# Kernel tuning notes

Hardware: AMD Instinct MI355X
Metric: run time of the kernel (lower is better)

## Reference

```python
import jax, jax.numpy as jnp
import numpy as np

N = 50000   # nodes
E = 600000  # edges
R = 8       # relations
B = 8       # bases
D = 128     # feature dim (in = hidden = out)
H = 4       # GAT heads
NEG = 0.1   # leaky_relu slope between layers
LN_EPS = 1e-5


def layer_norm(x, g, b):
    mu = jnp.mean(x, axis=-1, keepdims=True)
    var = jnp.mean(jnp.square(x - mu), axis=-1, keepdims=True)
    return (x - mu) * jax.lax.rsqrt(var + LN_EPS) * g + b


def rgcn(x, basis, comp, root, bias, src, dst, etype):
    # W[r] = sum_b comp[r,b] * basis[b]  -> [R, D, D]
    W = jnp.einsum('rb,bio->rio', comp, basis)
    h = jnp.einsum('ni,rio->rno', x, W)          # [R, N, D] per-relation transform
    msg = h[etype, src]                          # [E, D] gather per edge
    seg = etype.astype(jnp.int32) * N + dst      # (relation, dst) segment id
    deg = jax.ops.segment_sum(jnp.ones((src.shape[0],), x.dtype), seg, num_segments=R * N)
    inv = 1.0 / jnp.maximum(deg, 1.0)            # mean aggregation per relation
    out = jax.ops.segment_sum(msg * inv[seg][:, None], dst, num_segments=N)
    return out + x @ root + bias


def gat(x, W, a_src, a_dst, bias, src, dst):
    h = (x @ W).reshape(N, H, D)                 # [N, H, D]
    loop = jnp.arange(N, dtype=src.dtype)        # add self loops
    s2 = jnp.concatenate([src, loop])
    d2 = jnp.concatenate([dst, loop])
    hs = h[s2]                                   # [E+N, H, D]
    e = jnp.sum(hs * a_src, -1) + jnp.sum(h[d2] * a_dst, -1)   # [E+N, H]
    e = jax.nn.leaky_relu(e, 0.2)
    m = jax.ops.segment_max(e, d2, num_segments=N)              # stable softmax per dst
    ex = jnp.exp(e - m[d2])
    denom = jax.ops.segment_sum(ex, d2, num_segments=N)
    coef = ex / denom[d2]                        # [E+N, H]
    out = jax.ops.segment_sum(coef[..., None] * hs, d2, num_segments=N)  # [N, H, D]
    return jnp.mean(out, axis=1) + bias          # concat=False -> head mean


def setup_inputs():
    key = jax.random.key(0)
    ks = jax.random.split(key, 20)
    nrm = lambda k, shp, s=0.1: jax.random.normal(k, shp, dtype=jnp.float32) * s
    inp = {
        'x': jax.random.normal(ks[0], (N, D), dtype=jnp.float32),
        'edge_index': jax.random.randint(ks[1], (2, E), 0, N, dtype=jnp.int32),
        'edge_type': jax.random.randint(ks[2], (E,), 0, R, dtype=jnp.int32),
        'r0_basis': nrm(ks[3], (B, D, D)), 'r0_comp': nrm(ks[4], (R, B)),
        'r0_root': nrm(ks[5], (D, D)), 'r0_bias': jnp.zeros((D,), jnp.float32),
        'ln0_g': jnp.ones((D,), jnp.float32), 'ln0_b': jnp.zeros((D,), jnp.float32),
        'r1_basis': nrm(ks[6], (B, D, D)), 'r1_comp': nrm(ks[7], (R, B)),
        'r1_root': nrm(ks[8], (D, D)), 'r1_bias': jnp.zeros((D,), jnp.float32),
        'ln1_g': jnp.ones((D,), jnp.float32), 'ln1_b': jnp.zeros((D,), jnp.float32),
        'gat_w': nrm(ks[9], (D, H * D)), 'gat_asrc': nrm(ks[10], (H, D)),
        'gat_adst': nrm(ks[11], (H, D)), 'gat_bias': jnp.zeros((D,), jnp.float32),
        'ln2_g': jnp.ones((D,), jnp.float32), 'ln2_b': jnp.zeros((D,), jnp.float32),
        'r2_basis': nrm(ks[12], (B, D, D)), 'r2_comp': nrm(ks[13], (R, B)),
        'r2_root': nrm(ks[14], (D, D)), 'r2_bias': jnp.zeros((D,), jnp.float32),
    }
    return inp


def reference(x, edge_index, edge_type,
              r0_basis, r0_comp, r0_root, r0_bias, ln0_g, ln0_b,
              r1_basis, r1_comp, r1_root, r1_bias, ln1_g, ln1_b,
              gat_w, gat_asrc, gat_adst, gat_bias, ln2_g, ln2_b,
              r2_basis, r2_comp, r2_root, r2_bias):
    src, dst = edge_index[0], edge_index[1]
    h = rgcn(x, r0_basis, r0_comp, r0_root, r0_bias, src, dst, edge_type)
    h = jax.nn.leaky_relu(layer_norm(h, ln0_g, ln0_b), NEG)
    h = rgcn(h, r1_basis, r1_comp, r1_root, r1_bias, src, dst, edge_type)
    h = jax.nn.leaky_relu(layer_norm(h, ln1_g, ln1_b), NEG)
    h = gat(h, gat_w, gat_asrc, gat_adst, gat_bias, src, dst)
    h = jax.nn.leaky_relu(layer_norm(h, ln2_g, ln2_b), NEG)
    h = rgcn(h, r2_basis, r2_comp, r2_root, r2_bias, src, dst, edge_type)
    # F.normalize(p=2, dim=1)
    return h / jnp.maximum(jnp.linalg.norm(h, axis=1, keepdims=True), 1e-12)
```

## Files before the change

### kernel.cpp

```cpp
#include <hip/hip_runtime.h>
#include <hip/hip_bf16.h>

#define DD 128
#define NKEY8 8
#define LDA_AGG 1056
#define SRCM 0x00FFFFFF

using bf16x8 = __attribute__((ext_vector_type(8))) __bf16;
using f32x4  = __attribute__((ext_vector_type(4))) float;

__device__ __forceinline__ float leaky(float x, float s){ return x > 0.f ? x : s * x; }
__device__ __forceinline__ float bflo(unsigned u){ return __uint_as_float(u << 16); }
__device__ __forceinline__ float bfhi(unsigned u){ return __uint_as_float(u & 0xffff0000u); }
__device__ __forceinline__ unsigned bfpack(float x, float y){
  __hip_bfloat16 hx = __float2bfloat16(x), hy = __float2bfloat16(y);
  unsigned short ux = *reinterpret_cast<unsigned short*>(&hx);
  unsigned short uy = *reinterpret_cast<unsigned short*>(&hy);
  return (unsigned)ux | ((unsigned)uy << 16);
}

__global__ void k_hist(const int* __restrict__ dst, const int* __restrict__ et,
                       int* __restrict__ cnt, int E_){
  int e = blockIdx.x * 256 + threadIdx.x;
  if (e < E_) atomicAdd(&cnt[dst[e] * NKEY8 + et[e]], 1);
}

__global__ void k_scan1(const int* __restrict__ cnt, int* __restrict__ ptr,
                        int* __restrict__ part, int n){
  __shared__ int sm[256];
  int tid = threadIdx.x;
  int base = blockIdx.x * 1024 + tid * 4;
  int a0 = base + 0 < n ? cnt[base + 0] : 0;
  int a1 = base + 1 < n ? cnt[base + 1] : 0;
  int a2 = base + 2 < n ? cnt[base + 2] : 0;
  int a3 = base + 3 < n ? cnt[base + 3] : 0;
  int s = a0 + a1 + a2 + a3;
  sm[tid] = s; __syncthreads();
  for (int off = 1; off < 256; off <<= 1){
    int v = tid >= off ? sm[tid - off] : 0;
    __syncthreads(); sm[tid] += v; __syncthreads();
  }
  int ex = sm[tid] - s;
  if (tid == 255) part[blockIdx.x] = sm[255];
  if (base + 0 < n) ptr[base + 0] = ex;
  if (base + 1 < n) ptr[base + 1] = ex + a0;
  if (base + 2 < n) ptr[base + 2] = ex + a0 + a1;
  if (base + 3 < n) ptr[base + 3] = ex + a0 + a1 + a2;
}

__global__ void k_scan2(int* __restrict__ part, int nb){
  __shared__ int sm[512];
  int tid = threadIdx.x;
  int v = tid < nb ? part[tid] : 0;
  sm[tid] = v; __syncthreads();
  for (int off = 1; off < 512; off <<= 1){
    int u = tid >= off ? sm[tid - off] : 0;
    __syncthreads(); sm[tid] += u; __syncthreads();
  }
  if (tid < nb) part[tid] = sm[tid] - v;
}

__global__ void k_scan3(int* __restrict__ ptr, const int* __restrict__ part, int n, int E_){
  int i = blockIdx.x * 256 + threadIdx.x;
  if (i < n) ptr[i] += part[i >> 10];
  if (i == n) ptr[n] = E_;
}

__global__ void k_inv(const int* __restrict__ ptr, float* __restrict__ inv, int n){
  int i = blockIdx.x * 256 + threadIdx.x;
  if (i < n) inv[i] = 1.0f / fmaxf((float)(ptr[i + 1] - ptr[i]), 1.0f);
}

__global__ void k_scatter_pos(const int* __restrict__ src, const int* __restrict__ dst,
                              const int* __restrict__ et, int* __restrict__ run,
                              int* __restrict__ epk, int E_){
  int e = blockIdx.x * 256 + threadIdx.x;
  if (e >= E_) return;
  int r = et[e];
  int pos = atomicAdd(&run[dst[e] * NKEY8 + r], 1);
  epk[pos] = (r << 24) | src[e];
}

__global__ void k_cvt(const float* __restrict__ in, __hip_bfloat16* __restrict__ out, int n){
  int i = blockIdx.x * 256 + threadIdx.x;
  if (i < n) out[i] = __float2bfloat16(in[i]);
}

__global__ void k_makeW(const float* __restrict__ basis, const float* __restrict__ comp,
                        const float* __restrict__ root, __hip_bfloat16* __restrict__ Wp){
  int idx = blockIdx.x * 256 + threadIdx.x;
  int k = idx >> 7, n = idx & 127;
  float v;
  if (k < 1024){
    int r = k >> 7, i = k & 127;
    float s = 0.f;
    #pragma unroll
    for (int b = 0; b < 8; b++) s += comp[r * 8 + b] * basis[b * 16384 + i * 128 + n];
    v = s;
  } else {
    v = root[(k - 1024) * 128 + n];
  }
  int kt = k >> 5, kr = k & 31;
  int lane = (n & 15) | ((kr >> 3) << 4);
  int ii = kr & 7, nt = n >> 4;
  Wp[((size_t)(kt * 8 + nt) * 64 + lane) * 8 + ii] = __float2bfloat16(v);
}

__global__ void k_packGZ(const float* __restrict__ Wg, __hip_bfloat16* __restrict__ Wp){
  int idx = blockIdx.x * 256 + threadIdx.x;
  int k = idx >> 7, n = idx & 127;
  int h = k >> 7, i = k & 127;
  float v = Wg[(size_t)i * 512 + h * 128 + n];
  int kt = k >> 5, kr = k & 31;
  int lane = (n & 15) | ((kr >> 3) << 4);
  int ii = kr & 7, nt = n >> 4;
  Wp[((size_t)(kt * 8 + nt) * 64 + lane) * 8 + ii] = __float2bfloat16(v);
}

__global__ void k_valpha(const float* __restrict__ Wg, const float* __restrict__ a_src,
                         const float* __restrict__ a_dst, float* __restrict__ vT){
  int id = blockIdx.x * 256 + threadIdx.x;
  int sd = id >> 9, h = (id >> 7) & 3, i = id & 127;
  const float* a = (sd ? a_dst : a_src) + h * 128;
  const float* w = Wg + (size_t)i * 512 + h * 128;
  float s = 0.f;
  #pragma unroll 4
  for (int o = 0; o < 128; o++) s += w[o] * a[o];
  vT[(size_t)sd * 512 + h * 128 + i] = s;
}

__global__ void k_av(const __hip_bfloat16* __restrict__ xb, const float* __restrict__ vT,
                     float* __restrict__ aS, float* __restrict__ aD, int N_){
  int node = blockIdx.x * 4 + (threadIdx.x >> 6);
  if (node >= N_) return;
  int lane = threadIdx.x & 63;
  int h = lane >> 4, dg = lane & 15;
  uint4 u = *(const uint4*)(xb + (size_t)node * DD + dg * 8);
  const float* vs = vT + h * 128 + dg * 8;
  const float* vd = vT + 512 + h * 128 + dg * 8;
  float ss = 0.f, sd = 0.f;
  #pragma unroll
  for (int w = 0; w < 4; w++){
    unsigned uw = ((const unsigned*)&u)[w];
    float f0 = bflo(uw), f1 = bfhi(uw);
    ss += f0 * vs[w * 2] + f1 * vs[w * 2 + 1];
    sd += f0 * vd[w * 2] + f1 * vd[w * 2 + 1];
  }
  for (int o = 1; o < 16; o <<= 1){ ss += __shfl_xor(ss, o); sd += __shfl_xor(sd, o); }
  if (dg == 0){ aS[(size_t)node * 4 + h] = ss; aD[(size_t)node * 4 + h] = sd; }
}

__global__ void k_csr_agg(const int* __restrict__ ptr, const int* __restrict__ epk,
                          const float* __restrict__ inv, const __hip_bfloat16* __restrict__ xb,
                          __hip_bfloat16* __restrict__ agg, int N_){
  int w = threadIdx.x >> 6, lane = threadIdx.x & 63;
  int t = blockIdx.x * 4 + w;
  if (t >= N_) return;
  int beg = ptr[t * 8], end = ptr[t * 8 + 8];
  const __hip_bfloat16* xcol = xb + lane * 2;
  __hip_bfloat16* aggrow = agg + (size_t)t * LDA_AGG + lane * 2;
  const float* invrow = inv + (size_t)t * 8;
  float a0 = 0.f, a1 = 0.f;
  int cur = -1;
  unsigned written = 0;

#define CSR_FLUSH() { float iv = invrow[cur]; \
    *(unsigned*)(aggrow + cur * 128) = bfpack(a0 * iv, a1 * iv); \
    written |= (1u << cur); }
#define CSR_PROC(PK, U) { int r_ = (PK) >> 24; \
    if (r_ != cur){ if (cur >= 0){ CSR_FLUSH(); } cur = r_; a0 = 0.f; a1 = 0.f; } \
    a0 += bflo(U); a1 += bfhi(U); }

  int e = beg;
  for (; e + 4 <= end; e += 4){
    int pk0 = epk[e], pk1 = epk[e + 1], pk2 = epk[e + 2], pk3 = epk[e + 3];
    unsigned u0 = *(const unsigned*)(xcol + (size_t)(pk0 & SRCM) * DD);
    unsigned u1 = *(const unsigned*)(xcol + (size_t)(pk1 & SRCM) * DD);
    unsigned u2 = *(const unsigned*)(xcol + (size_t)(pk2 & SRCM) * DD);
    unsigned u3 = *(const unsigned*)(xcol + (size_t)(pk3 & SRCM) * DD);
    CSR_PROC(pk0, u0); CSR_PROC(pk1, u1); CSR_PROC(pk2, u2); CSR_PROC(pk3, u3);
  }
  for (; e < end; e++){
    int pk0 = epk[e];
    unsigned u0 = *(const unsigned*)(xcol + (size_t)(pk0 & SRCM) * DD);
    CSR_PROC(pk0, u0);
  }
  if (cur >= 0){ CSR_FLUSH(); }
  #pragma unroll
  for (int r = 0; r < 8; r++)
    if (!(written & (1u << r))) *(unsigned*)(aggrow + r * 128) = 0u;
#undef CSR_PROC
#undef CSR_FLUSH
}

__global__ void k_zagg(const int* __restrict__ ptr, const int* __restrict__ epk,
                       const float* __restrict__ cf, const float* __restrict__ cfS,
                       const float* __restrict__ den, const __hip_bfloat16* __restrict__ xb,
                       __hip_bfloat16* __restrict__ z, int N_){
  int w = threadIdx.x >> 6, lane = threadIdx.x & 63;
  int t = blockIdx.x * 4 + w;
  if (t >= N_) return;
  int dg = lane & 31, ep = lane >> 5;
  int beg = ptr[t * 8], end = ptr[t * 8 + 8];
  float acc[4][4];
  #pragma unroll
  for (int h = 0; h < 4; h++)
    #pragma unroll
    for (int j = 0; j < 4; j++) acc[h][j] = 0.f;
  const __hip_bfloat16* xbase = xb + dg * 4;
  for (int e = beg + ep; e < end; e += 2){
    int s = epk[e] & SRCM;
    uint2 v = *(const uint2*)(xbase + (size_t)s * DD);
    float4 c = *(const float4*)(cf + (size_t)e * 4);
    float f0 = bflo(v.x), f1 = bfhi(v.x), f2 = bflo(v.y), f3 = bfhi(v.y);
    const float* cp = (const float*)&c;
    #pragma unroll
    for (int h = 0; h < 4; h++){
      acc[h][0] += cp[h] * f0; acc[h][1] += cp[h] * f1;
      acc[h][2] += cp[h] * f2; acc[h][3] += cp[h] * f3;
    }
  }
  #pragma unroll
  for (int h = 0; h < 4; h++)
    #pragma unroll
    for (int j = 0; j < 4; j++) acc[h][j] += __shfl_xor(acc[h][j], 32);
  if (ep == 0){
    uint2 v = *(const uint2*)(xbase + (size_t)t * DD);
    float f0 = bflo(v.x), f1 = bfhi(v.x), f2 = bflo(v.y), f3 = bfhi(v.y);
    float4 cs = *(const float4*)(cfS + (size_t)t * 4);
    float4 dn = *(const float4*)(den + (size_t)t * 4);
    const float* csp = (const float*)&cs;
    const float* dnp = (const float*)&dn;
    #pragma unroll
    for (int h = 0; h < 4; h++){
      float sc = 0.25f / dnp[h];
      float y0 = (acc[h][0] + csp[h] * f0) * sc;
      float y1 = (acc[h][1] + csp[h] * f1) * sc;
      float y2 = (acc[h][2] + csp[h] * f2) * sc;
      float y3 = (acc[h][3] + csp[h] * f3) * sc;
      uint2 o; o.x = bfpack(y0, y1); o.y = bfpack(y2, y3);
      *(uint2*)(z + (size_t)t * 512 + h * 128 + dg * 4) = o;
    }
  }
}

template<int MODE>
__launch_bounds__(256)
__global__ void k_gemm_mfma(const __hip_bfloat16* __restrict__ A1, int lda1, int K1,
                            const __hip_bfloat16* __restrict__ A2, int K2,
                            int M, const __hip_bfloat16* __restrict__ Bp, int ntt,
                            const float* __restrict__ bias,
                            const float* __restrict__ ln_g, const float* __restrict__ ln_b,
                            float* __restrict__ Cf, __hip_bfloat16* __restrict__ Cb,
                            int ldc){
  int wave = threadIdx.x >> 6, lane = threadIdx.x & 63;
  int nt0 = blockIdx.y << 3;
  int mbase = blockIdx.x * 128 + wave * 32;
  int r0 = min(mbase + (lane & 15), M - 1);
  int r1 = min(mbase + 16 + (lane & 15), M - 1);
  int koff = (lane >> 4) << 3;
  f32x4 acc[2][8];
  #pragma unroll
  for (int i = 0; i < 2; i++)
    #pragma unroll
    for (int j = 0; j < 8; j++) acc[i][j] = (f32x4){0.f, 0.f, 0.f, 0.f};

  int ktile = 0;
  {
    const __hip_bfloat16* a0p = A1 + (size_t)r0 * lda1 + koff;
    const __hip_bfloat16* a1p = A1 + (size_t)r1 * lda1 + koff;
    for (int k0 = 0; k0 < K1; k0 += 32, ++ktile){
      bf16x8 a0 = *(const bf16x8*)(a0p + k0);
      bf16x8 a1 = *(const bf16x8*)(a1p + k0);
      const bf16x8* bfr = (const bf16x8*)(Bp + (((size_t)ktile * ntt + nt0) * 64 + lane) * 8);
      #pragma unroll
      for (int nt = 0; nt < 8; nt++){
        bf16x8 b = bfr[(size_t)nt * 64];
        acc[0][nt] = __builtin_amdgcn_mfma_f32_16x16x32_bf16(a0, b, acc[0][nt], 0, 0, 0);
        acc[1][nt] = __builtin_amdgcn_mfma_f32_16x16x32_bf16(a1, b, acc[1][nt], 0, 0, 0);
      }
    }
  }
  if (A2){
    const __hip_bfloat16* a0p = A2 + (size_t)r0 * DD + koff;
    const __hip_bfloat16* a1p = A2 + (size_t)r1 * DD + koff;
    for (int k0 = 0; k0 < K2; k0 += 32, ++ktile){
      bf16x8 a0 = *(const bf16x8*)(a0p + k0);
      bf16x8 a1 = *(const bf16x8*)(a1p + k0);
      const bf16x8* bfr = (const bf16x8*)(Bp + (((size_t)ktile * ntt + nt0) * 64 + lane) * 8);
      #pragma unroll
      for (int nt = 0; nt < 8; nt++){
        bf16x8 b = bfr[(size_t)nt * 64];
        acc[0][nt] = __builtin_amdgcn_mfma_f32_16x16x32_bf16(a0, b, acc[0][nt], 0, 0, 0);
        acc[1][nt] = __builtin_amdgcn_mfma_f32_16x16x32_bf16(a1, b, acc[1][nt], 0, 0, 0);
      }
    }
  }

  const int colb = lane & 15;
  const int lq = lane >> 4;

  float bias8[8], g8[8], b8[8];
  #pragma unroll
  for (int nt = 0; nt < 8; nt++){
    int c = (nt << 4) + colb;
    bias8[nt] = bias ? bias[c] : 0.f;
    if (MODE == 1){ g8[nt] = ln_g[c]; b8[nt] = ln_b[c]; }
  }

  #pragma unroll
  for (int mt = 0; mt < 2; mt++){
    #pragma unroll
    for (int j = 0; j < 4; j++){
      int row = mbase + mt * 16 + lq * 4 + j;
      if (MODE == 1){
        float v[8]; float s = 0.f;
        #pragma unroll
        for (int nt = 0; nt < 8; nt++){ v[nt] = acc[mt][nt][j] + bias8[nt]; s += v[nt]; }
        #pragma unroll
        for (int o = 1; o < 16; o <<= 1) s += __shfl_xor(s, o);
        float mu = s * (1.f / 128.f);
        float q = 0.f;
        #pragma unroll
        for (int nt = 0; nt < 8; nt++){ float dd = v[nt] - mu; q += dd * dd; }
        #pragma unroll
        for (int o = 1; o < 16; o <<= 1) q += __shfl_xor(q, o);
        float rstd = rsqrtf(q * (1.f / 128.f) + 1e-5f);
        if (row < M){
          #pragma unroll
          for (int nt = 0; nt < 8; nt++){
            float y = leaky((v[nt] - mu) * rstd * g8[nt] + b8[nt], 0.1f);
            Cb[(size_t)row * ldc + (nt << 4) + colb] = __float2bfloat16(y);
          }
        }
      } else {
        float v[8]; float q = 0.f;
        #pragma unroll
        for (int nt = 0; nt < 8; nt++){ v[nt] = acc[mt][nt][j] + bias8[nt]; q += v[nt] * v[nt]; }
        #pragma unroll
        for (int o = 1; o < 16; o <<= 1) q += __shfl_xor(q, o);
        float sc = 1.0f / fmaxf(sqrtf(q), 1e-12f);
        if (row < M){
          #pragma unroll
          for (int nt = 0; nt < 8; nt++)
            Cf[(size_t)row * ldc + (nt << 4) + colb] = v[nt] * sc;
        }
      }
    }
  }
}

__global__ void k_gat_coef(const int* __restrict__ ptr, const int* __restrict__ epk,
                           const float* __restrict__ aS, const float* __restrict__ aD,
                           float* __restrict__ cf, float* __restrict__ cfS,
                           float* __restrict__ den, int N_){
  int id = blockIdx.x * 256 + threadIdx.x;
  int t = id >> 2, h = id & 3;
  if (t >= N_) return;
  int beg = ptr[t * 8], end = ptr[t * 8 + 8];
  float adh = aD[(size_t)t * 4 + h];
  float ash = aS[(size_t)t * 4 + h];
  float selfe = leaky(ash + adh, 0.2f);
  float m = selfe;
  for (int e = beg; e < end; e++){
    int s = epk[e] & SRCM;
    m = fmaxf(m, leaky(aS[(size_t)s * 4 + h] + adh, 0.2f));
  }
  float sv = __expf(selfe - m);
  cfS[(size_t)t * 4 + h] = sv;
  float d = sv;
  for (int e = beg; e < end; e++){
    int s = epk[e] & SRCM;
    float x = __expf(leaky(aS[(size_t)s * 4 + h] + adh, 0.2f) - m);
    cf[(size_t)e * 4 + h] = x;
    d += x;
  }
  den[(size_t)t * 4 + h] = d;
}

extern "C" void kernel_launch(void* const* d_in, const int* in_sizes, int n_in,
                              void* d_out, int out_size, void* d_ws, size_t ws_size,
                              hipStream_t stream){
  const float* x       = (const float*)d_in[0];
  const int*   ei      = (const int*)d_in[1];
  const int*   et      = (const int*)d_in[2];
  const float* r0_basis= (const float*)d_in[3];  const float* r0_comp = (const float*)d_in[4];
  const float* r0_root = (const float*)d_in[5];  const float* r0_bias = (const float*)d_in[6];
  const float* ln0_g   = (const float*)d_in[7];  const float* ln0_b   = (const float*)d_in[8];
  const float* r1_basis= (const float*)d_in[9];  const float* r1_comp = (const float*)d_in[10];
  const float* r1_root = (const float*)d_in[11]; const float* r1_bias = (const float*)d_in[12];
  const float* ln1_g   = (const float*)d_in[13]; const float* ln1_b   = (const float*)d_in[14];
  const float* gat_w   = (const float*)d_in[15]; const float* gat_asrc= (const float*)d_in[16];
  const float* gat_adst= (const float*)d_in[17]; const float* gat_bias= (const float*)d_in[18];
  const float* ln2_g   = (const float*)d_in[19]; const float* ln2_b   = (const float*)d_in[20];
  const float* r2_basis= (const float*)d_in[21]; const float* r2_comp = (const float*)d_in[22];
  const float* r2_root = (const float*)d_in[23]; const float* r2_bias = (const float*)d_in[24];

  const int N_ = in_sizes[0] / DD;
  const int E_ = in_sizes[2];
  const int NK = N_ * NKEY8;
  const int* src = ei;
  const int* dst = ei + E_;
  float* T2 = (float*)d_out;

  char* wp_ = (char*)d_ws;
  auto alloc = [&](size_t b)->void*{ void* p = wp_; wp_ += (b + 255) & ~(size_t)255; return p; };
  __hip_bfloat16* agg16 = (__hip_bfloat16*)alloc((size_t)N_ * LDA_AGG * 2);
  __hip_bfloat16* xb16  = (__hip_bfloat16*)alloc((size_t)N_ * DD * 2);
  float*          inv   = (float*)alloc((size_t)NK * 4);
  int*            ptrb  = (int*)alloc((size_t)(NK + 1) * 4);
  int*            cnt   = (int*)alloc((size_t)NK * 4);
  int*            run   = (int*)alloc((size_t)NK * 4);
  int*            epk   = (int*)alloc((size_t)E_ * 4);
  int*            part  = (int*)alloc(512 * 4);
  float*          aS    = (float*)alloc((size_t)N_ * 4 * 4);
  float*          aD    = (float*)alloc((size_t)N_ * 4 * 4);
  float*          cf    = (float*)alloc((size_t)E_ * 4 * 4);
  float*          cfS   = (float*)alloc((size_t)N_ * 4 * 4);
  float*          den   = (float*)alloc((size_t)N_ * 4 * 4);
  float*          vT    = (float*)alloc((size_t)2 * 512 * 4);
  __hip_bfloat16* Wp    = (__hip_bfloat16*)alloc((size_t)1152 * 128 * 2);
  __hip_bfloat16* WpZ   = (__hip_bfloat16*)alloc((size_t)512 * 128 * 2);
  if ((size_t)(wp_ - (char*)d_ws) > ws_size) return;
  __hip_bfloat16* z16 = agg16;

  const int Mb = (N_ + 127) / 128;
  const int nScanB = (NK + 1023) / 1024;

  hipMemsetAsync(cnt, 0, (size_t)NK * 4, stream);
  k_hist<<<(E_ + 255) / 256, 256, 0, stream>>>(dst, et, cnt, E_);
  k_scan1<<<nScanB, 256, 0, stream>>>(cnt, ptrb, part, NK);
  k_scan2<<<1, 512, 0, stream>>>(part, nScanB);
  k_scan3<<<(NK + 1 + 255) / 256, 256, 0, stream>>>(ptrb, part, NK, E_);
  k_inv<<<(NK + 255) / 256, 256, 0, stream>>>(ptrb, inv, NK);
  hipMemcpyAsync(run, ptrb, (size_t)NK * 4, hipMemcpyDeviceToDevice, stream);
  k_scatter_pos<<<(E_ + 255) / 256, 256, 0, stream>>>(src, dst, et, run, epk, E_);
  k_cvt<<<(N_ * DD + 255) / 256, 256, 0, stream>>>(x, xb16, N_ * DD);

  k_makeW<<<576, 256, 0, stream>>>(r0_basis, r0_comp, r0_root, Wp);
  k_csr_agg<<<(N_ + 3) / 4, 256, 0, stream>>>(ptrb, epk, inv, xb16, agg16, N_);
  k_gemm_mfma<1><<<dim3(Mb, 1), 256, 0, stream>>>(agg16, LDA_AGG, 1024, xb16, 128, N_, Wp, 8,
      r0_bias, ln0_g, ln0_b, nullptr, xb16, DD);

  k_makeW<<<576, 256, 0, stream>>>(r1_basis, r1_comp, r1_root, Wp);
  k_csr_agg<<<(N_ + 3) / 4, 256, 0, stream>>>(ptrb, epk, inv, xb16, agg16, N_);
  k_gemm_mfma<1><<<dim3(Mb, 1), 256, 0, stream>>>(agg16, LDA_AGG, 1024, xb16, 128, N_, Wp, 8,
      r1_bias, ln1_g, ln1_b, nullptr, xb16, DD);

  k_valpha<<<4, 256, 0, stream>>>(gat_w, gat_asrc, gat_adst, vT);
  k_packGZ<<<256, 256, 0, stream>>>(gat_w, WpZ);
  k_av<<<(N_ + 3) / 4, 256, 0, stream>>>(xb16, vT, aS, aD, N_);
  k_gat_coef<<<(N_ * 4 + 255) / 256, 256, 0, stream>>>(ptrb, epk, aS, aD, cf, cfS, den, N_);
  k_zagg<<<(N_ + 3) / 4, 256, 0, stream>>>(ptrb, epk, cf, cfS, den, xb16, z16, N_);
  k_gemm_mfma<1><<<dim3(Mb, 1), 256, 0, stream>>>(z16, 512, 512, nullptr, 0, N_, WpZ, 8,
      gat_bias, ln2_g, ln2_b, nullptr, xb16, DD);

  k_makeW<<<576, 256, 0, stream>>>(r2_basis, r2_comp, r2_root, Wp);
  k_csr_agg<<<(N_ + 3) / 4, 256, 0, stream>>>(ptrb, epk, inv, xb16, agg16, N_);
  k_gemm_mfma<3><<<dim3(Mb, 1), 256, 0, stream>>>(agg16, LDA_AGG, 1024, xb16, 128, N_, Wp, 8,
      r2_bias, nullptr, nullptr, T2, nullptr, DD);
}
```

Before: 464.0 us.

## Fold run-copy into k_inv, unroll CSR gather by 8, cache GAT logits

```diff
diff --git a/kernel.cpp b/kernel.cpp
--- a/kernel.cpp
+++ b/kernel.cpp
@@ -66,9 +66,14 @@
   if (i == n) ptr[n] = E_;
 }
 
-__global__ void k_inv(const int* __restrict__ ptr, float* __restrict__ inv, int n){
+__global__ void k_inv(const int* __restrict__ ptr, float* __restrict__ inv,
+                      int* __restrict__ run, int n){
   int i = blockIdx.x * 256 + threadIdx.x;
-  if (i < n) inv[i] = 1.0f / fmaxf((float)(ptr[i + 1] - ptr[i]), 1.0f);
+  if (i < n){
+    int p = ptr[i];
+    inv[i] = 1.0f / fmaxf((float)(ptr[i + 1] - p), 1.0f);
+    run[i] = p;
+  }
 }
 
 __global__ void k_scatter_pos(const int* __restrict__ src, const int* __restrict__ dst,
@@ -172,6 +177,20 @@
     a0 += bflo(U); a1 += bfhi(U); }
 
   int e = beg;
+  for (; e + 8 <= end; e += 8){
+    int pk0 = epk[e],     pk1 = epk[e + 1], pk2 = epk[e + 2], pk3 = epk[e + 3];
+    int pk4 = epk[e + 4], pk5 = epk[e + 5], pk6 = epk[e + 6], pk7 = epk[e + 7];
+    unsigned u0 = *(const unsigned*)(xcol + (size_t)(pk0 & SRCM) * DD);
+    unsigned u1 = *(const unsigned*)(xcol + (size_t)(pk1 & SRCM) * DD);
+    unsigned u2 = *(const unsigned*)(xcol + (size_t)(pk2 & SRCM) * DD);
+    unsigned u3 = *(const unsigned*)(xcol + (size_t)(pk3 & SRCM) * DD);
+    unsigned u4 = *(const unsigned*)(xcol + (size_t)(pk4 & SRCM) * DD);
+    unsigned u5 = *(const unsigned*)(xcol + (size_t)(pk5 & SRCM) * DD);
+    unsigned u6 = *(const unsigned*)(xcol + (size_t)(pk6 & SRCM) * DD);
+    unsigned u7 = *(const unsigned*)(xcol + (size_t)(pk7 & SRCM) * DD);
+    CSR_PROC(pk0, u0); CSR_PROC(pk1, u1); CSR_PROC(pk2, u2); CSR_PROC(pk3, u3);
+    CSR_PROC(pk4, u4); CSR_PROC(pk5, u5); CSR_PROC(pk6, u6); CSR_PROC(pk7, u7);
+  }
   for (; e + 4 <= end; e += 4){
     int pk0 = epk[e], pk1 = epk[e + 1], pk2 = epk[e + 2], pk3 = epk[e + 3];
     unsigned u0 = *(const unsigned*)(xcol + (size_t)(pk0 & SRCM) * DD);
@@ -364,14 +383,15 @@
   float m = selfe;
   for (int e = beg; e < end; e++){
     int s = epk[e] & SRCM;
-    m = fmaxf(m, leaky(aS[(size_t)s * 4 + h] + adh, 0.2f));
+    float l = leaky(aS[(size_t)s * 4 + h] + adh, 0.2f);
+    cf[(size_t)e * 4 + h] = l;
+    m = fmaxf(m, l);
   }
   float sv = __expf(selfe - m);
   cfS[(size_t)t * 4 + h] = sv;
   float d = sv;
   for (int e = beg; e < end; e++){
-    int s = epk[e] & SRCM;
-    float x = __expf(leaky(aS[(size_t)s * 4 + h] + adh, 0.2f) - m);
+    float x = __expf(cf[(size_t)e * 4 + h] - m);
     cf[(size_t)e * 4 + h] = x;
     d += x;
   }
@@ -432,8 +452,7 @@
   k_scan1<<<nScanB, 256, 0, stream>>>(cnt, ptrb, part, NK);
   k_scan2<<<1, 512, 0, stream>>>(part, nScanB);
   k_scan3<<<(NK + 1 + 255) / 256, 256, 0, stream>>>(ptrb, part, NK, E_);
-  k_inv<<<(NK + 255) / 256, 256, 0, stream>>>(ptrb, inv, NK);
-  hipMemcpyAsync(run, ptrb, (size_t)NK * 4, hipMemcpyDeviceToDevice, stream);
+  k_inv<<<(NK + 255) / 256, 256, 0, stream>>>(ptrb, inv, run, NK);
   k_scatter_pos<<<(E_ + 255) / 256, 256, 0, stream>>>(src, dst, et, run, epk, E_);
   k_cvt<<<(N_ * DD + 255) / 256, 256, 0, stream>>>(x, xb16, N_ * DD);
 
```

Result: faster. 452.5 us (-2.5%).
